# Kernel optimization log

Measured on AMD Instinct MI355X. Metric: run time of the kernel, lower is better.

The kernel has to match this reference:

```python
import jax, jax.numpy as jnp
import numpy as np

UNITS = 256
INNER_ITERS = 1
INNER_LR = [0.01]
LN_EPS = 1e-3  # keras LayerNormalization default epsilon
B, L, F = 512, 128, 128


def _encoder(W1, b1, W2, b2, z):
    # keras 'gelu' activation is exact (approximate=False)
    h = jax.nn.gelu(z @ W1 + b1, approximate=False)
    return h @ W2 + b2


def _layer_norm(z, g, b):
    m = jnp.mean(z, axis=-1, keepdims=True)
    v = jnp.var(z, axis=-1, keepdims=True)
    return g * (z - m) / jnp.sqrt(v + LN_EPS) + b


def setup_inputs():
    U = UNITS
    key = jax.random.key(0)
    ks = jax.random.split(key, 12)
    s = 0.02
    return {
        "inputs": jax.random.normal(ks[0], (B, F), jnp.float32),
        "prev_hidden": jax.random.normal(ks[1], (B, U), jnp.float32),
        "sequence_buffer": jax.random.normal(ks[2], (B, L, U), jnp.float32),
        "Wp": jax.random.normal(ks[3], (F, U)) * s, "bp": jnp.zeros((U,)),
        "Wphi": jax.random.normal(ks[4], (U, U)) * s, "bphi": jnp.zeros((U,)),
        "Wpsi": jax.random.normal(ks[5], (U, U)) * s, "bpsi": jnp.zeros((U,)),
        "W1": jax.random.normal(ks[6], (U, 4 * U)) * s, "b1": jnp.zeros((4 * U,)),
        "W2": jax.random.normal(ks[7], (4 * U, U)) * s, "b2": jnp.zeros((U,)),
        "Wg": jax.random.normal(ks[8], (U, U)) * s, "g_bias": jnp.zeros((U,)),
        "ln_g": jnp.ones((U,)), "ln_b": jnp.zeros((U,)),
        "Wh": jax.random.normal(ks[9], (U, U)) * s, "h_bias": jnp.zeros((U,)),
    }


def reference(inputs, prev_hidden, sequence_buffer, Wp, bp, Wphi, bphi, Wpsi, bpsi,
              W1, b1, W2, b2, Wg, g_bias, ln_g, ln_b, Wh, h_bias):
    U = UNITS
    bsz = inputs.shape[0]
    # input projection (F != units)
    proj = inputs @ Wp + bp                                   # [B, U]
    # shift buffer, append projected input
    buf = jnp.concatenate([sequence_buffer[:, 1:, :], proj[:, None, :]], axis=1)  # [B, L, U]
    x = buf[:, :-1, :].reshape(-1, U)                         # [B*(L-1), U]
    y = buf[:, 1:, :].reshape(-1, U)
    phi = x @ Wphi + bphi

    params = (W1, b1, W2, b2)

    def inner_loss(p):
        rec = _layer_norm(_encoder(*p, phi) @ Wg + g_bias, ln_g, ln_b)
        return jnp.mean(jnp.square(rec - y)), rec

    rec = None
    for it in range(INNER_ITERS):
        (_, rec), grads = jax.value_and_grad(inner_loss, has_aux=True)(params)
        lr = INNER_LR[min(it, len(INNER_LR) - 1)]
        params = tuple(p - lr * g for p, g in zip(params, grads))

    psi = buf[:, -1, :] @ Wpsi + bpsi                         # [B, U]
    contrib = jnp.mean(rec.reshape(bsz, -1, U), axis=1)       # [B, U]
    # psi path uses the UPDATED inner-encoder weights
    out = (_encoder(*params, psi) + contrib) @ Wh + h_bias    # [B, U]
    return out, buf
```

## Files before the change

### kernel.cpp

```cpp
#include <hip/hip_runtime.h>
#include <cmath>

typedef __bf16 bf16;
typedef __attribute__((ext_vector_type(8))) __bf16 bf16x8;
typedef __attribute__((ext_vector_type(4))) __bf16 bf16x4v;
typedef __attribute__((ext_vector_type(4))) float f32x4;
typedef __attribute__((ext_vector_type(2))) unsigned int u32x2;

constexpr int NROWS = 512 * 127;
constexpr float LR = 0.01f;
constexpr float INV_NU = 1.f / (65024.f * 256.f);

__device__ __forceinline__ float sigf(float x) {
  return 1.f / (1.f + __expf(-1.702f * x));
}
__device__ __forceinline__ float gelu_fast(float x) { return x * sigf(x); }
__device__ __forceinline__ float dgelu_fast(float x) {
  float s = sigf(x);
  return s * (1.f + 1.702f * x * (1.f - s));
}
__device__ __forceinline__ bf16x8 gelu8f(bf16x8 v) {
  bf16x8 o;
#pragma unroll
  for (int i = 0; i < 8; i++) o[i] = (bf16)gelu_fast((float)v[i]);
  return o;
}

__device__ __forceinline__ void gload16(const bf16* g, const bf16* lds) {
  __builtin_amdgcn_global_load_lds(
      (const __attribute__((address_space(1))) unsigned int*)(size_t)(const void*)g,
      (__attribute__((address_space(3))) unsigned int*)(unsigned)(size_t)(const void*)lds,
      16, 0, 0);
}

__device__ __forceinline__ int xcd_lin() {
  int p = ((int)blockIdx.z * (int)gridDim.y + (int)blockIdx.y) * (int)gridDim.x + (int)blockIdx.x;
  const int total = (int)gridDim.x * (int)gridDim.y * (int)gridDim.z;
  if (!(total & 7)) p = (p & 7) * (total >> 3) + (p >> 3);
  return p;
}

template <int EPI>
__global__ __launch_bounds__(256, 4) void gemm6_k(
    const bf16* __restrict__ A, const bf16* __restrict__ Bt,
    const float* __restrict__ bias, void* __restrict__ out0,
    void* __restrict__ out1, const bf16* __restrict__ aux,
    int M, int N, int K) {
  __shared__ __align__(16) bf16 As[2][128 * 32];
  __shared__ __align__(16) bf16 Bs[2][128 * 32];
  const int t = threadIdx.x;
  const int p = xcd_lin();
  const int bn = (p % (int)gridDim.x) * 128;
  const int bm = (p / (int)gridDim.x) * 128;
  const int lane = t & 63, w = t >> 6;
  const int wr = w >> 1, wc = w & 1;

  f32x4 acc[4][4];
#pragma unroll
  for (int mi = 0; mi < 4; mi++)
#pragma unroll
    for (int ni = 0; ni < 4; ni++) {
      f32x4 z = {0.f, 0.f, 0.f, 0.f};
      acc[mi][ni] = z;
    }

  const int lr = lane >> 2;
  const int csw = (lane & 3) ^ (lr & 3);
  const bf16* aBase = A + (size_t)(bm + 32 * w + lr) * K + csw * 8;
  const bf16* bBase = Bt + (size_t)(bn + 32 * w + lr) * K + csw * 8;

  const int ml = lane & 15, g = lane >> 4;
  const int c0 = g ^ (ml & 3);

  const int nt = K >> 5;
#pragma unroll
  for (int i = 0; i < 2; i++) {
    gload16(aBase + (size_t)(16 * i) * K, As[0] + (32 * w + 16 * i) * 32);
    gload16(bBase + (size_t)(16 * i) * K, Bs[0] + (32 * w + 16 * i) * 32);
  }

  for (int tt = 0; tt < nt; tt++) {
    const int cur = tt & 1;
    if (tt + 1 < nt) {
      const int ko = (tt + 1) * 32;
#pragma unroll
      for (int i = 0; i < 2; i++) {
        gload16(aBase + (size_t)(16 * i) * K + ko, As[cur ^ 1] + (32 * w + 16 * i) * 32);
        gload16(bBase + (size_t)(16 * i) * K + ko, Bs[cur ^ 1] + (32 * w + 16 * i) * 32);
      }
      asm volatile("s_waitcnt vmcnt(4)" ::: "memory");
    } else {
      asm volatile("s_waitcnt vmcnt(0)" ::: "memory");
    }
    __builtin_amdgcn_s_barrier();
    __builtin_amdgcn_sched_barrier(0);

    bf16x8 af[4], bfr[4];
#pragma unroll
    for (int mi = 0; mi < 4; mi++) {
      const int m = wr * 64 + mi * 16 + ml;
      const int n = wc * 64 + mi * 16 + ml;
      af[mi] = *(const bf16x8*)&As[cur][m * 32 + c0 * 8];
      bfr[mi] = *(const bf16x8*)&Bs[cur][n * 32 + c0 * 8];
    }
#pragma unroll
    for (int mi = 0; mi < 4; mi++)
#pragma unroll
      for (int ni = 0; ni < 4; ni++)
        acc[mi][ni] = __builtin_amdgcn_mfma_f32_16x16x32_bf16(
            bfr[ni], af[mi], acc[mi][ni], 0, 0, 0);
    __builtin_amdgcn_s_barrier();
  }

  const int g4 = (lane >> 4) << 2;
#pragma unroll
  for (int mi = 0; mi < 4; mi++) {
    const int m = bm + wr * 64 + mi * 16 + ml;
#pragma unroll
    for (int ni = 0; ni < 4; ni++) {
      const int n0 = bn + wc * 64 + ni * 16 + g4;
      f32x4 v = acc[mi][ni];
      if (bias) {
        const float4 bv = *(const float4*)(bias + n0);
        v[0] += bv.x; v[1] += bv.y; v[2] += bv.z; v[3] += bv.w;
      }
      const size_t idx = (size_t)m * N + n0;
      if constexpr (EPI == 0) {
        *(float4*)((float*)out0 + idx) = make_float4(v[0], v[1], v[2], v[3]);
      } else if constexpr (EPI == 1) {
        bf16x4v o;
#pragma unroll
        for (int j = 0; j < 4; j++) o[j] = (bf16)v[j];
        *(bf16x4v*)((bf16*)out0 + idx) = o;
      } else if constexpr (EPI == 2) {
        bf16x4v od, oh;
#pragma unroll
        for (int j = 0; j < 4; j++) {
          float s = sigf(v[j]);
          oh[j] = (bf16)(v[j] * s);
          od[j] = (bf16)(s * (1.f + 1.702f * v[j] * (1.f - s)));
        }
        *(bf16x4v*)((bf16*)out0 + idx) = od;
        *(bf16x4v*)((bf16*)out1 + idx) = oh;
      } else if constexpr (EPI == 3) {
        bf16x4v o;
#pragma unroll
        for (int j = 0; j < 4; j++) o[j] = (bf16)gelu_fast(v[j]);
        *(bf16x4v*)((bf16*)out0 + idx) = o;
      } else if constexpr (EPI == 5) {
        const bf16x4v a4 = *(const bf16x4v*)(aux + idx);
        bf16x4v o;
#pragma unroll
        for (int j = 0; j < 4; j++) o[j] = (bf16)(v[j] * dgelu_fast((float)a4[j]));
        *(bf16x4v*)((bf16*)out0 + idx) = o;
      } else if constexpr (EPI == 6) {
        const bf16x4v a4 = *(const bf16x4v*)(aux + idx);
        bf16x4v o;
#pragma unroll
        for (int j = 0; j < 4; j++) o[j] = (bf16)(v[j] * (float)a4[j]);
        *(bf16x4v*)((bf16*)out0 + idx) = o;
      } else if constexpr (EPI == 7) {
        *(float4*)((float*)out0 + idx) = make_float4(v[0], v[1], v[2], v[3]);
        bf16x4v o;
#pragma unroll
        for (int j = 0; j < 4; j++) o[j] = (bf16)v[j];
        *(bf16x4v*)((bf16*)out1 + idx) = o;
      } else {
        const float4 c4 = *(const float4*)((const float*)aux + idx);
        bf16x4v o;
        o[0] = (bf16)(v[0] + c4.x); o[1] = (bf16)(v[1] + c4.y);
        o[2] = (bf16)(v[2] + c4.z); o[3] = (bf16)(v[3] + c4.w);
        *(bf16x4v*)((bf16*)out0 + idx) = o;
      }
    }
  }
}

template <int EPI, bool GA>
__global__ __launch_bounds__(256) void gemm_k(
    const bf16* __restrict__ A, const bf16* __restrict__ Bt,
    const float* __restrict__ bias, void* __restrict__ out0,
    void* __restrict__ out1, const bf16* __restrict__ aux,
    int M, int N, int K) {
  __shared__ bf16 As[128][40];
  __shared__ bf16 Bs[128][40];
  const int t = threadIdx.x;
  const int bm = blockIdx.x * 128, bn = blockIdx.y * 128;
  const int lane = t & 63, w = t >> 6;
  const int wr = w >> 1, wc = w & 1;

  f32x4 acc[4][4];
#pragma unroll
  for (int mi = 0; mi < 4; mi++)
#pragma unroll
    for (int ni = 0; ni < 4; ni++) {
      f32x4 z = {0.f, 0.f, 0.f, 0.f};
      acc[mi][ni] = z;
    }
  const int r2 = t >> 2;
  const int c8 = (t & 3) * 8;

  for (int kt = 0; kt < K; kt += 32) {
    __syncthreads();
    {
      bf16x8 a0 = *(const bf16x8*)(A + (size_t)(bm + r2) * K + kt + c8);
      bf16x8 a1 = *(const bf16x8*)(A + (size_t)(bm + r2 + 64) * K + kt + c8);
      bf16x8 b0 = *(const bf16x8*)(Bt + (size_t)(bn + r2) * K + kt + c8);
      bf16x8 b1 = *(const bf16x8*)(Bt + (size_t)(bn + r2 + 64) * K + kt + c8);
      if constexpr (GA) { a0 = gelu8f(a0); a1 = gelu8f(a1); }
      *(bf16x8*)&As[r2][c8] = a0;
      *(bf16x8*)&As[r2 + 64][c8] = a1;
      *(bf16x8*)&Bs[r2][c8] = b0;
      *(bf16x8*)&Bs[r2 + 64][c8] = b1;
    }
    __syncthreads();
    bf16x8 af[4], bfr[4];
#pragma unroll
    for (int mi = 0; mi < 4; mi++)
      af[mi] = *(const bf16x8*)&As[wr * 64 + mi * 16 + (lane & 15)][(lane >> 4) * 8];
#pragma unroll
    for (int ni = 0; ni < 4; ni++)
      bfr[ni] = *(const bf16x8*)&Bs[wc * 64 + ni * 16 + (lane & 15)][(lane >> 4) * 8];
#pragma unroll
    for (int mi = 0; mi < 4; mi++)
#pragma unroll
      for (int ni = 0; ni < 4; ni++)
        acc[mi][ni] = __builtin_amdgcn_mfma_f32_16x16x32_bf16(af[mi], bfr[ni], acc[mi][ni], 0, 0, 0);
  }

#pragma unroll
  for (int ni = 0; ni < 4; ni++) {
    const int col = bn + wc * 64 + ni * 16 + (lane & 15);
    const float bv = bias ? bias[col] : 0.f;
#pragma unroll
    for (int mi = 0; mi < 4; mi++) {
      const int rb = bm + wr * 64 + mi * 16 + ((lane >> 4) << 2);
#pragma unroll
      for (int r = 0; r < 4; r++) {
        float v = acc[mi][ni][r] + bv;
        size_t idx = (size_t)(rb + r) * N + col;
        if constexpr (EPI == 1) {
          ((bf16*)out0)[idx] = (bf16)v;
        } else {
          ((float*)out0)[idx] = v;
        }
      }
    }
  }
}

template <bool GELU_A>
__global__ __launch_bounds__(256) void tgemm4_k(
    const bf16* __restrict__ Asrc, const bf16* __restrict__ Bsrc,
    float* __restrict__ outP, int M, int N, int ldA, int ldB, int K) {
  __shared__ __align__(16) bf16 As[2][4736];
  __shared__ __align__(16) bf16 Bs[2][4736];
  const int t = threadIdx.x;
  const int p = xcd_lin();
  const int gx = (int)gridDim.x, gy = (int)gridDim.y;
  const int bm = (p % gx) * 128;
  const int bn = ((p / gx) % gy) * 128;
  const int zc = p / (gx * gy);
  const int r0 = zc * 1024;
  const int rows = (K - r0 < 1024) ? (K - r0) : 1024;
  const int nt = rows >> 5;
  const int lane = t & 63, w = t >> 6, wr = w >> 1, wc = w & 1;

  f32x4 acc[4][4];
#pragma unroll
  for (int mi = 0; mi < 4; mi++)
#pragma unroll
    for (int ni = 0; ni < 4; ni++) {
      f32x4 z = {0.f, 0.f, 0.f, 0.f};
      acc[mi][ni] = z;
    }

  const bool isB = t >= 128;
  const int srow = (t & 127) >> 4;
  const int scol = (t & 15) * 8;
  const int sms = (t & 15) >> 1;
  const int shalf = (t & 1) * 8;
  const bf16* src = isB ? Bsrc : Asrc;
  const int ld = isB ? ldB : ldA;
  const int bx = isB ? bn : bm;
  const int sidx = sms * 592 + srow * 16 + shalf;

  const unsigned abase = (unsigned)(size_t)(void*)As;
  const unsigned bbase = (unsigned)(size_t)(void*)Bs;
  const int g = lane >> 4;
  const int ml = lane & 15;
  const unsigned acol0 = abase + 2u * (unsigned)((wr * 4) * 592 + g * 144 + ml);
  const unsigned bcol0 = bbase + 2u * (unsigned)((wc * 4) * 592 + g * 144 + ml);

  auto ldrow = [&](int kt, int ll) {
    return *(const bf16x8*)(src + (size_t)(r0 + kt + srow + ll * 8) * ld + bx + scol);
  };
  auto wrbuf = [&](bf16* dst, bf16x8* stg) {
#pragma unroll
    for (int ll = 0; ll < 4; ll++) {
      bf16x8 v = stg[ll];
      if constexpr (GELU_A) { if (!isB) v = gelu8f(v); }
      *(bf16x8*)&dst[sidx + ll * 144] = v;
    }
  };

  bf16x8 stg[4];
#pragma unroll
  for (int ll = 0; ll < 4; ll++) stg[ll] = ldrow(0, ll);
  wrbuf(isB ? Bs[0] : As[0], stg);
  __syncthreads();

  for (int tt = 0; tt < nt; tt++) {
    const int cur = tt & 1;
    if (tt + 1 < nt) {
#pragma unroll
      for (int ll = 0; ll < 4; ll++) stg[ll] = ldrow((tt + 1) * 32, ll);
    }
    const unsigned boff = (unsigned)cur * (4736u * 2u);
    union FR { u32x2 pr[2]; bf16x8 v; };
    FR af[4], bfr[4];
#pragma unroll
    for (int mi = 0; mi < 4; mi++) {
      const unsigned a = acol0 + boff + (unsigned)(mi * 1184);
      asm volatile("ds_read_b64_tr_b16 %0, %1" : "=v"(af[mi].pr[0]) : "v"(a));
      asm volatile("ds_read_b64_tr_b16 %0, %1 offset:128" : "=v"(af[mi].pr[1]) : "v"(a));
    }
#pragma unroll
    for (int ni = 0; ni < 4; ni++) {
      const unsigned b = bcol0 + boff + (unsigned)(ni * 1184);
      asm volatile("ds_read_b64_tr_b16 %0, %1" : "=v"(bfr[ni].pr[0]) : "v"(b));
      asm volatile("ds_read_b64_tr_b16 %0, %1 offset:128" : "=v"(bfr[ni].pr[1]) : "v"(b));
    }
    asm volatile("s_waitcnt lgkmcnt(0)" ::: "memory");
    __builtin_amdgcn_sched_barrier(0);

#pragma unroll
    for (int mi = 0; mi < 4; mi++)
#pragma unroll
      for (int ni = 0; ni < 4; ni++)
        acc[mi][ni] = __builtin_amdgcn_mfma_f32_16x16x32_bf16(
            bfr[ni].v, af[mi].v, acc[mi][ni], 0, 0, 0);

    if (tt + 1 < nt) wrbuf(isB ? Bs[cur ^ 1] : As[cur ^ 1], stg);
    __syncthreads();
  }

  float* o = outP + (size_t)zc * M * N;
  const int g4 = (lane >> 4) << 2;
#pragma unroll
  for (int mi = 0; mi < 4; mi++) {
    const int m = bm + wr * 64 + mi * 16 + ml;
#pragma unroll
    for (int ni = 0; ni < 4; ni++) {
      const int n0 = bn + wc * 64 + ni * 16 + g4;
      f32x4 v = acc[mi][ni];
      *(float4*)(o + (size_t)m * N + n0) = make_float4(v[0], v[1], v[2], v[3]);
    }
  }
}

__global__ void prep_k(const float* inputs, const float* Wp, const float* Wphi,
                       const float* W1, const float* W2, const float* Wg,
                       const float* Wpsi, const float* Wh,
                       bf16* inb, bf16* WpT, bf16* WphiT, bf16* W1T, bf16* W2T,
                       bf16* WgT, bf16* Wgb, bf16* W2b, bf16* WpsiT, bf16* WhT) {
  int i = blockIdx.x * 256 + threadIdx.x;
  if (i < 65536) {
    inb[i] = (bf16)inputs[i];
  } else if ((i -= 65536) < 32768) {
    int u = i >> 7, f = i & 127;
    WpT[i] = (bf16)Wp[f * 256 + u];
  } else if ((i -= 32768) < 65536) {
    int n = i >> 8, k = i & 255;
    WphiT[i] = (bf16)Wphi[k * 256 + n];
  } else if ((i -= 65536) < 262144) {
    int h = i >> 8, u = i & 255;
    W1T[i] = (bf16)W1[u * 1024 + h];
  } else if ((i -= 262144) < 262144) {
    int u = i >> 10, h = i & 1023;
    W2T[i] = (bf16)W2[h * 256 + u];
  } else if ((i -= 262144) < 65536) {
    int n = i >> 8, k = i & 255;
    WgT[i] = (bf16)Wg[k * 256 + n];
  } else if ((i -= 65536) < 65536) {
    Wgb[i] = (bf16)Wg[i];
  } else if ((i -= 65536) < 262144) {
    W2b[i] = (bf16)W2[i];
  } else if ((i -= 262144) < 65536) {
    int n = i >> 8, k = i & 255;
    WpsiT[i] = (bf16)Wpsi[k * 256 + n];
  } else if ((i -= 65536) < 65536) {
    int n = i >> 8, k = i & 255;
    WhT[i] = (bf16)Wh[k * 256 + n];
  }
}

__global__ void bzg_k(const float* __restrict__ b2, const float* __restrict__ Wg,
                      const float* __restrict__ gbias, float* __restrict__ bzg) {
  const int n = threadIdx.x;
  float s = gbias[n];
  for (int j = 0; j < 256; j++) s += b2[j] * Wg[j * 256 + n];
  bzg[n] = s;
}

__global__ void xcast_k(const float* __restrict__ seq, bf16* __restrict__ xb) {
  int v8 = blockIdx.x * 256 + threadIdx.x;
  int r = v8 >> 5, c8 = (v8 & 31) * 8;
  int b = r / 127, t = r - b * 127;
  const float* src = seq + ((size_t)(b * 128 + t + 1)) * 256 + c8;
  float4 v0 = *(const float4*)(src);
  float4 v1 = *(const float4*)(src + 4);
  bf16x8 o;
  o[0] = (bf16)v0.x; o[1] = (bf16)v0.y; o[2] = (bf16)v0.z; o[3] = (bf16)v0.w;
  o[4] = (bf16)v1.x; o[5] = (bf16)v1.y; o[6] = (bf16)v1.z; o[7] = (bf16)v1.w;
  *(bf16x8*)(xb + (size_t)r * 256 + c8) = o;
}

__global__ void bufwrite_k(const float* __restrict__ seq, const float* __restrict__ proj,
                           float* __restrict__ buf) {
  int i = blockIdx.x * 256 + threadIdx.x;
  int b = i >> 13, rem = i & 8191;
  int j = rem >> 6, c4 = (rem & 63) * 4;
  float4 v;
  if (j < 127)
    v = *(const float4*)(seq + ((size_t)(b * 128 + j + 1)) * 256 + c4);
  else
    v = *(const float4*)(proj + (size_t)b * 256 + c4);
  *(float4*)(buf + ((size_t)(b * 128 + j)) * 256 + c4) = v;
}

__global__ __launch_bounds__(256) void ln_k(const bf16* zin, bf16* dzout,
                                            const float* __restrict__ seq,
                                            const float* __restrict__ proj,
                                            const float* __restrict__ lng,
                                            const float* __restrict__ lnb,
                                            bf16* __restrict__ rec) {
  const int w = threadIdx.x >> 6, lane = threadIdx.x & 63;
  const int r = blockIdx.x * 4 + w;
  const int b = r / 127, tt = r - b * 127;
  typedef __attribute__((ext_vector_type(4))) __bf16 bf16x4;
  bf16x4 zv = *(const bf16x4*)(zin + (size_t)r * 256 + lane * 4);
  float z0 = (float)zv[0], z1 = (float)zv[1], z2 = (float)zv[2], z3 = (float)zv[3];
  float s1 = z0 + z1 + z2 + z3;
  float s2 = z0 * z0 + z1 * z1 + z2 * z2 + z3 * z3;
  for (int m = 1; m < 64; m <<= 1) { s1 += __shfl_xor(s1, m); s2 += __shfl_xor(s2, m); }
  const float mean = s1 * (1.f / 256.f);
  const float var = s2 * (1.f / 256.f) - mean * mean;
  const float rs = rsqrtf(var + 1e-3f);
  const float4 gv = *(const float4*)(lng + lane * 4);
  const float4 bv = *(const float4*)(lnb + lane * 4);
  const float* ysrc = (tt < 126) ? (seq + ((size_t)(b * 128 + tt + 2)) * 256)
                                 : (proj + (size_t)b * 256);
  const float4 yv = *(const float4*)(ysrc + lane * 4);
  float xh0 = (z0 - mean) * rs, xh1 = (z1 - mean) * rs, xh2 = (z2 - mean) * rs, xh3 = (z3 - mean) * rs;
  float r0 = gv.x * xh0 + bv.x, r1 = gv.y * xh1 + bv.y, r2 = gv.z * xh2 + bv.z, r3 = gv.w * xh3 + bv.w;
  float u0 = 2.f * (r0 - yv.x) * INV_NU * gv.x;
  float u1 = 2.f * (r1 - yv.y) * INV_NU * gv.y;
  float u2 = 2.f * (r2 - yv.z) * INV_NU * gv.z;
  float u3 = 2.f * (r3 - yv.w) * INV_NU * gv.w;
  float t1 = u0 + u1 + u2 + u3;
  float t2 = u0 * xh0 + u1 * xh1 + u2 * xh2 + u3 * xh3;
  for (int m = 1; m < 64; m <<= 1) { t1 += __shfl_xor(t1, m); t2 += __shfl_xor(t2, m); }
  const float mu = t1 * (1.f / 256.f), mux = t2 * (1.f / 256.f);
  bf16x4 ro, dzo;
  ro[0] = (bf16)r0; ro[1] = (bf16)r1; ro[2] = (bf16)r2; ro[3] = (bf16)r3;
  dzo[0] = (bf16)((u0 - mu - xh0 * mux) * rs);
  dzo[1] = (bf16)((u1 - mu - xh1 * mux) * rs);
  dzo[2] = (bf16)((u2 - mu - xh2 * mux) * rs);
  dzo[3] = (bf16)((u3 - mu - xh3 * mux) * rs);
  *(bf16x4*)(rec + (size_t)r * 256 + lane * 4) = ro;
  *(bf16x4*)(dzout + (size_t)r * 256 + lane * 4) = dzo;
}

__global__ void colsum_k(const bf16* __restrict__ src, float* __restrict__ part, int C) {
  const int col = blockIdx.x * 256 + threadIdx.x;
  const int ch = blockIdx.y;
  float s = 0.f;
  const int rbeg = ch * 1016;
  for (int rr = rbeg; rr < rbeg + 1016; rr++) s += (float)src[(size_t)rr * C + col];
  part[(size_t)ch * C + col] = s;
}

__global__ void contrib_k(const bf16* __restrict__ rec, float* __restrict__ contrib) {
  const int b = blockIdx.x, u = threadIdx.x;
  float s = 0.f;
  for (int t = 0; t < 127; t++) s += (float)rec[((size_t)b * 127 + t) * 256 + u];
  contrib[b * 256 + u] = s * (1.f / 127.f);
}

__global__ void update2_k(const float* __restrict__ pW2, const float* __restrict__ pdb2,
                          const float* __restrict__ W2, const float* __restrict__ b2,
                          bf16* __restrict__ W2pT, float* __restrict__ b2p) {
  int idx = blockIdx.x * 256 + threadIdx.x;
  if (idx < 262144) {
    float s = 0.f;
    for (int z = 0; z < 64; z++) s += pW2[(size_t)z * 262144 + idx];
    int h = idx >> 8, u = idx & 255;
    W2pT[(size_t)u * 1024 + h] = (bf16)(W2[idx] - LR * s);
  } else {
    int u = idx - 262144;
    float s = 0.f;
    for (int c = 0; c < 64; c++) s += pdb2[c * 256 + u];
    b2p[u] = b2[u] - LR * s;
  }
}

__global__ void update1_k(const float* __restrict__ pW1, const float* __restrict__ pdb1,
                          const float* __restrict__ W1, const float* __restrict__ b1,
                          bf16* __restrict__ W1pT, float* __restrict__ b1p) {
  int idx = blockIdx.x * 256 + threadIdx.x;
  if (idx < 262144) {
    float s = 0.f;
    for (int z = 0; z < 64; z++) s += pW1[(size_t)z * 262144 + idx];
    int u = idx >> 10, h = idx & 1023;
    W1pT[(size_t)h * 256 + u] = (bf16)(W1[idx] - LR * s);
  } else {
    int h = idx - 262144;
    float s = 0.f;
    for (int c = 0; c < 64; c++) s += pdb1[c * 1024 + h];
    b1p[h] = b1[h] - LR * s;
  }
}

extern "C" void kernel_launch(void* const* d_in, const int* in_sizes, int n_in,
                              void* d_out, int out_size, void* d_ws, size_t ws_size,
                              hipStream_t stream) {
  const float* inputs = (const float*)d_in[0];
  const float* seq = (const float*)d_in[2];
  const float* Wp = (const float*)d_in[3];
  const float* bp = (const float*)d_in[4];
  const float* Wphi = (const float*)d_in[5];
  const float* bphi = (const float*)d_in[6];
  const float* Wpsi = (const float*)d_in[7];
  const float* bpsi = (const float*)d_in[8];
  const float* W1 = (const float*)d_in[9];
  const float* b1 = (const float*)d_in[10];
  const float* W2 = (const float*)d_in[11];
  const float* b2 = (const float*)d_in[12];
  const float* Wg = (const float*)d_in[13];
  const float* gbias = (const float*)d_in[14];
  const float* lng = (const float*)d_in[15];
  const float* lnb = (const float*)d_in[16];
  const float* Wh = (const float*)d_in[17];
  const float* hbias = (const float*)d_in[18];

  float* out = (float*)d_out;
  float* buf = out + 131072;
  float* pW2 = buf;
  float* pW1 = buf;

  char* wptr = (char*)d_ws;
  auto alloc = [&](size_t bytes) {
    char* p = wptr;
    wptr += (bytes + 255) & ~(size_t)255;
    return p;
  };
  bf16* inb   = (bf16*)alloc(65536 * 2);
  bf16* WpT   = (bf16*)alloc(32768 * 2);
  bf16* WphiT = (bf16*)alloc(65536 * 2);
  bf16* W1T   = (bf16*)alloc(262144 * 2);
  bf16* W2T   = (bf16*)alloc(262144 * 2);
  bf16* WgT   = (bf16*)alloc(65536 * 2);
  bf16* Wgb   = (bf16*)alloc(65536 * 2);
  bf16* W2b   = (bf16*)alloc(262144 * 2);
  bf16* WpsiT = (bf16*)alloc(65536 * 2);
  bf16* WhT   = (bf16*)alloc(65536 * 2);
  bf16* WzgT  = (bf16*)alloc(262144 * 2);
  float* bzg  = (float*)alloc(256 * 4);
  bf16* W1pT  = (bf16*)alloc(262144 * 2);
  bf16* W2pT  = (bf16*)alloc(262144 * 2);
  float* b1p  = (float*)alloc(1024 * 4);
  float* b2p  = (float*)alloc(256 * 4);
  float* proj = (float*)alloc(131072 * 4);
  bf16* projb = (bf16*)alloc(131072 * 2);
  float* pdb2 = (float*)alloc(64 * 256 * 4);
  float* pdb1 = (float*)alloc(64 * 1024 * 4);
  bf16* psib  = (bf16*)alloc(131072 * 2);
  bf16* hpb   = (bf16*)alloc(524288 * 2);
  float* contrib = (float*)alloc(131072 * 4);
  bf16* finb  = (bf16*)alloc(131072 * 2);
  const size_t NU = (size_t)NROWS * 256;
  const size_t NH = (size_t)NROWS * 1024;
  bf16* xz     = (bf16*)alloc(NU * 2);
  bf16* phi    = (bf16*)alloc(NU * 2);
  bf16* a1b    = (bf16*)alloc(NH * 2);
  bf16* encden = (bf16*)alloc(NU * 2);
  const bool useH = ws_size >= (size_t)((char*)wptr - (char*)d_ws) + NH * 2 + 4096;
  bf16* hbuf = useH ? (bf16*)alloc(NH * 2) : nullptr;

  prep_k<<<4736, 256, 0, stream>>>(inputs, Wp, Wphi, W1, W2, Wg, Wpsi, Wh,
                                   inb, WpT, WphiT, W1T, W2T, WgT, Wgb, W2b, WpsiT, WhT);
  gemm6_k<1><<<dim3(8, 2), 256, 0, stream>>>(WgT, W2b, nullptr, WzgT, nullptr, nullptr, 256, 1024, 256);
  bzg_k<<<1, 256, 0, stream>>>(b2, Wg, gbias, bzg);
  xcast_k<<<8128, 256, 0, stream>>>(seq, xz);
  gemm6_k<7><<<dim3(2, 4), 256, 0, stream>>>(inb, WpT, bp, proj, projb, nullptr, 512, 256, 128);
  gemm6_k<1><<<dim3(2, 508), 256, 0, stream>>>(xz, WphiT, bphi, phi, nullptr, nullptr, NROWS, 256, 256);
  if (useH)
    gemm6_k<2><<<dim3(8, 508), 256, 0, stream>>>(phi, W1T, b1, a1b, hbuf, nullptr, NROWS, 1024, 256);
  else
    gemm6_k<1><<<dim3(8, 508), 256, 0, stream>>>(phi, W1T, b1, a1b, nullptr, nullptr, NROWS, 1024, 256);
  if (useH)
    gemm6_k<1><<<dim3(2, 508), 256, 0, stream>>>(hbuf, WzgT, bzg, xz, nullptr, nullptr, NROWS, 256, 1024);
  else
    gemm_k<1, true><<<dim3(508, 2), 256, 0, stream>>>(a1b, WzgT, bzg, xz, nullptr, nullptr, NROWS, 256, 1024);
  ln_k<<<16256, 256, 0, stream>>>(xz, xz, seq, proj, lng, lnb, encden);
  contrib_k<<<512, 256, 0, stream>>>(encden, contrib);
  gemm6_k<1><<<dim3(2, 508), 256, 0, stream>>>(xz, Wgb, nullptr, encden, nullptr, nullptr, NROWS, 256, 256);
  colsum_k<<<dim3(1, 64), 256, 0, stream>>>(encden, pdb2, 256);
  if (useH)
    tgemm4_k<false><<<dim3(8, 2, 64), 256, 0, stream>>>(hbuf, encden, pW2, 1024, 256, 1024, 256, NROWS);
  else
    tgemm4_k<true><<<dim3(8, 2, 64), 256, 0, stream>>>(a1b, encden, pW2, 1024, 256, 1024, 256, NROWS);
  update2_k<<<1025, 256, 0, stream>>>(pW2, pdb2, W2, b2, W2pT, b2p);
  if (useH)
    gemm6_k<6><<<dim3(8, 508), 256, 0, stream>>>(encden, W2b, nullptr, a1b, nullptr, a1b, NROWS, 1024, 256);
  else
    gemm6_k<5><<<dim3(8, 508), 256, 0, stream>>>(encden, W2b, nullptr, a1b, nullptr, a1b, NROWS, 1024, 256);
  colsum_k<<<dim3(4, 64), 256, 0, stream>>>(a1b, pdb1, 1024);
  tgemm4_k<false><<<dim3(2, 8, 64), 256, 0, stream>>>(phi, a1b, pW1, 256, 1024, 256, 1024, NROWS);
  update1_k<<<1028, 256, 0, stream>>>(pW1, pdb1, W1, b1, W1pT, b1p);
  bufwrite_k<<<16384, 256, 0, stream>>>(seq, proj, buf);
  gemm6_k<1><<<dim3(2, 4), 256, 0, stream>>>(projb, WpsiT, bpsi, psib, nullptr, nullptr, 512, 256, 256);
  gemm6_k<3><<<dim3(8, 4), 256, 0, stream>>>(psib, W1pT, b1p, hpb, nullptr, nullptr, 512, 1024, 256);
  gemm6_k<8><<<dim3(2, 4), 256, 0, stream>>>(hpb, W2pT, b2p, finb, nullptr, (const bf16*)contrib, 512, 256, 1024);
  gemm6_k<0><<<dim3(2, 4), 256, 0, stream>>>(finb, WhT, hbias, out, nullptr, nullptr, 512, 256, 256);
}
```

Measured before the change: 889.7 us.

## Drop materialized GELU buffer; fuse GELU into pipelined Zg GEMM load

Removes the optional separate GELU activation buffer (hbuf) and its extra 65024x1024 bf16 write and reads. GELU is recomputed on the fly when loading A tiles, both in a new double-buffered, swizzled GEMM kernel for the Wzg projection and in the weight-gradient GEMM. The new kernel also uses an XCD-aware block order, async B loads and vectorized epilogue stores. It saves memory traffic at the cost of recomputing GELU twice per element.

```diff
diff --git a/kernel.cpp b/kernel.cpp
--- a/kernel.cpp
+++ b/kernel.cpp
@@ -176,16 +176,18 @@
   }
 }
 
-template <int EPI, bool GA>
-__global__ __launch_bounds__(256) void gemm_k(
+template <int EPI>
+__global__ __launch_bounds__(256, 4) void gemm7_k(
     const bf16* __restrict__ A, const bf16* __restrict__ Bt,
     const float* __restrict__ bias, void* __restrict__ out0,
     void* __restrict__ out1, const bf16* __restrict__ aux,
     int M, int N, int K) {
-  __shared__ bf16 As[128][40];
-  __shared__ bf16 Bs[128][40];
+  __shared__ __align__(16) bf16 As[2][128 * 32];
+  __shared__ __align__(16) bf16 Bs[2][128 * 32];
   const int t = threadIdx.x;
-  const int bm = blockIdx.x * 128, bn = blockIdx.y * 128;
+  const int p = xcd_lin();
+  const int bn = (p % (int)gridDim.x) * 128;
+  const int bm = (p / (int)gridDim.x) * 128;
   const int lane = t & 63, w = t >> 6;
   const int wr = w >> 1, wc = w & 1;
 
@@ -197,53 +199,80 @@
       f32x4 z = {0.f, 0.f, 0.f, 0.f};
       acc[mi][ni] = z;
     }
-  const int r2 = t >> 2;
-  const int c8 = (t & 3) * 8;
-
-  for (int kt = 0; kt < K; kt += 32) {
+
+  const int lr = lane >> 2;
+  const int csw = (lane & 3) ^ (lr & 3);
+  const bf16* aBase = A + (size_t)(bm + 32 * w + lr) * K + csw * 8;
+  const bf16* bBase = Bt + (size_t)(bn + 32 * w + lr) * K + csw * 8;
+  const int awoff = (32 * w + lr) * 32 + (lane & 3) * 8;
+
+  const int ml = lane & 15, g = lane >> 4;
+  const int c0 = g ^ (ml & 3);
+
+  const int nt = K >> 5;
+  {
+    bf16x8 av0 = *(const bf16x8*)aBase;
+    bf16x8 av1 = *(const bf16x8*)(aBase + (size_t)16 * K);
+    gload16(bBase, Bs[0] + (32 * w) * 32);
+    gload16(bBase + (size_t)16 * K, Bs[0] + (32 * w + 16) * 32);
+    *(bf16x8*)&As[0][awoff] = gelu8f(av0);
+    *(bf16x8*)&As[0][awoff + 512] = gelu8f(av1);
+  }
+  __syncthreads();
+
+  bf16x8 av0, av1;
+  for (int tt = 0; tt < nt; tt++) {
+    const int cur = tt & 1;
+    if (tt + 1 < nt) {
+      const int ko = (tt + 1) * 32;
+      gload16(bBase + ko, Bs[cur ^ 1] + (32 * w) * 32);
+      gload16(bBase + (size_t)16 * K + ko, Bs[cur ^ 1] + (32 * w + 16) * 32);
+      av0 = *(const bf16x8*)(aBase + ko);
+      av1 = *(const bf16x8*)(aBase + (size_t)16 * K + ko);
+    }
+
+    bf16x8 af[4], bfr[4];
+#pragma unroll
+    for (int mi = 0; mi < 4; mi++) {
+      const int m = wr * 64 + mi * 16 + ml;
+      const int n = wc * 64 + mi * 16 + ml;
+      af[mi] = *(const bf16x8*)&As[cur][m * 32 + c0 * 8];
+      bfr[mi] = *(const bf16x8*)&Bs[cur][n * 32 + c0 * 8];
+    }
+#pragma unroll
+    for (int mi = 0; mi < 4; mi++)
+#pragma unroll
+      for (int ni = 0; ni < 4; ni++)
+        acc[mi][ni] = __builtin_amdgcn_mfma_f32_16x16x32_bf16(
+            bfr[ni], af[mi], acc[mi][ni], 0, 0, 0);
+
+    if (tt + 1 < nt) {
+      *(bf16x8*)&As[cur ^ 1][awoff] = gelu8f(av0);
+      *(bf16x8*)&As[cur ^ 1][awoff + 512] = gelu8f(av1);
+    }
     __syncthreads();
-    {
-      bf16x8 a0 = *(const bf16x8*)(A + (size_t)(bm + r2) * K + kt + c8);
-      bf16x8 a1 = *(const bf16x8*)(A + (size_t)(bm + r2 + 64) * K + kt + c8);
-      bf16x8 b0 = *(const bf16x8*)(Bt + (size_t)(bn + r2) * K + kt + c8);
-      bf16x8 b1 = *(const bf16x8*)(Bt + (size_t)(bn + r2 + 64) * K + kt + c8);
-      if constexpr (GA) { a0 = gelu8f(a0); a1 = gelu8f(a1); }
-      *(bf16x8*)&As[r2][c8] = a0;
-      *(bf16x8*)&As[r2 + 64][c8] = a1;
-      *(bf16x8*)&Bs[r2][c8] = b0;
-      *(bf16x8*)&Bs[r2 + 64][c8] = b1;
-    }
-    __syncthreads();
-    bf16x8 af[4], bfr[4];
-#pragma unroll
-    for (int mi = 0; mi < 4; mi++)
-      af[mi] = *(const bf16x8*)&As[wr * 64 + mi * 16 + (lane & 15)][(lane >> 4) * 8];
-#pragma unroll
-    for (int ni = 0; ni < 4; ni++)
-      bfr[ni] = *(const bf16x8*)&Bs[wc * 64 + ni * 16 + (lane & 15)][(lane >> 4) * 8];
-#pragma unroll
-    for (int mi = 0; mi < 4; mi++)
-#pragma unroll
-      for (int ni = 0; ni < 4; ni++)
-        acc[mi][ni] = __builtin_amdgcn_mfma_f32_16x16x32_bf16(af[mi], bfr[ni], acc[mi][ni], 0, 0, 0);
-  }
-
-#pragma unroll
-  for (int ni = 0; ni < 4; ni++) {
-    const int col = bn + wc * 64 + ni * 16 + (lane & 15);
-    const float bv = bias ? bias[col] : 0.f;
-#pragma unroll
-    for (int mi = 0; mi < 4; mi++) {
-      const int rb = bm + wr * 64 + mi * 16 + ((lane >> 4) << 2);
-#pragma unroll
-      for (int r = 0; r < 4; r++) {
-        float v = acc[mi][ni][r] + bv;
-        size_t idx = (size_t)(rb + r) * N + col;
-        if constexpr (EPI == 1) {
-          ((bf16*)out0)[idx] = (bf16)v;
-        } else {
-          ((float*)out0)[idx] = v;
-        }
+  }
+
+  const int g4 = (lane >> 4) << 2;
+#pragma unroll
+  for (int mi = 0; mi < 4; mi++) {
+    const int m = bm + wr * 64 + mi * 16 + ml;
+#pragma unroll
+    for (int ni = 0; ni < 4; ni++) {
+      const int n0 = bn + wc * 64 + ni * 16 + g4;
+      f32x4 v = acc[mi][ni];
+      if (bias) {
+        const float4 bv = *(const float4*)(bias + n0);
+        v[0] += bv.x; v[1] += bv.y; v[2] += bv.z; v[3] += bv.w;
+      }
+      const size_t idx = (size_t)m * N + n0;
+      if constexpr (EPI == 0) {
+        *(float4*)((float*)out0 + idx) = make_float4(v[0], v[1], v[2], v[3]);
+      } else {
+        bf16x4v o;
+#pragma unroll
+        for (int j = 0; j < 4; j++) o[j] = (bf16)v[j];
+        *(bf16x4v*)((bf16*)out0 + idx) = o;
       }
     }
   }
@@ -585,8 +614,6 @@
   bf16* phi    = (bf16*)alloc(NU * 2);
   bf16* a1b    = (bf16*)alloc(NH * 2);
   bf16* encden = (bf16*)alloc(NU * 2);
-  const bool useH = ws_size >= (size_t)((char*)wptr - (char*)d_ws) + NH * 2 + 4096;
-  bf16* hbuf = useH ? (bf16*)alloc(NH * 2) : nullptr;
 
   prep_k<<<4736, 256, 0, stream>>>(inputs, Wp, Wphi, W1, W2, Wg, Wpsi, Wh,
                                    inb, WpT, WphiT, W1T, W2T, WgT, Wgb, W2b, WpsiT, WhT);
@@ -595,27 +622,15 @@
   xcast_k<<<8128, 256, 0, stream>>>(seq, xz);
   gemm6_k<7><<<dim3(2, 4), 256, 0, stream>>>(inb, WpT, bp, proj, projb, nullptr, 512, 256, 128);
   gemm6_k<1><<<dim3(2, 508), 256, 0, stream>>>(xz, WphiT, bphi, phi, nullptr, nullptr, NROWS, 256, 256);
-  if (useH)
-    gemm6_k<2><<<dim3(8, 508), 256, 0, stream>>>(phi, W1T, b1, a1b, hbuf, nullptr, NROWS, 1024, 256);
-  else
-    gemm6_k<1><<<dim3(8, 508), 256, 0, stream>>>(phi, W1T, b1, a1b, nullptr, nullptr, NROWS, 1024, 256);
-  if (useH)
-    gemm6_k<1><<<dim3(2, 508), 256, 0, stream>>>(hbuf, WzgT, bzg, xz, nullptr, nullptr, NROWS, 256, 1024);
-  else
-    gemm_k<1, true><<<dim3(508, 2), 256, 0, stream>>>(a1b, WzgT, bzg, xz, nullptr, nullptr, NROWS, 256, 1024);
+  gemm6_k<1><<<dim3(8, 508), 256, 0, stream>>>(phi, W1T, b1, a1b, nullptr, nullptr, NROWS, 1024, 256);
+  gemm7_k<1><<<dim3(2, 508), 256, 0, stream>>>(a1b, WzgT, bzg, xz, nullptr, nullptr, NROWS, 256, 1024);
   ln_k<<<16256, 256, 0, stream>>>(xz, xz, seq, proj, lng, lnb, encden);
   contrib_k<<<512, 256, 0, stream>>>(encden, contrib);
   gemm6_k<1><<<dim3(2, 508), 256, 0, stream>>>(xz, Wgb, nullptr, encden, nullptr, nullptr, NROWS, 256, 256);
   colsum_k<<<dim3(1, 64), 256, 0, stream>>>(encden, pdb2, 256);
-  if (useH)
-    tgemm4_k<false><<<dim3(8, 2, 64), 256, 0, stream>>>(hbuf, encden, pW2, 1024, 256, 1024, 256, NROWS);
-  else
-    tgemm4_k<true><<<dim3(8, 2, 64), 256, 0, stream>>>(a1b, encden, pW2, 1024, 256, 1024, 256, NROWS);
+  tgemm4_k<true><<<dim3(8, 2, 64), 256, 0, stream>>>(a1b, encden, pW2, 1024, 256, 1024, 256, NROWS);
   update2_k<<<1025, 256, 0, stream>>>(pW2, pdb2, W2, b2, W2pT, b2p);
-  if (useH)
-    gemm6_k<6><<<dim3(8, 508), 256, 0, stream>>>(encden, W2b, nullptr, a1b, nullptr, a1b, NROWS, 1024, 256);
-  else
-    gemm6_k<5><<<dim3(8, 508), 256, 0, stream>>>(encden, W2b, nullptr, a1b, nullptr, a1b, NROWS, 1024, 256);
+  gemm6_k<5><<<dim3(8, 508), 256, 0, stream>>>(encden, W2b, nullptr, a1b, nullptr, a1b, NROWS, 1024, 256);
   colsum_k<<<dim3(4, 64), 256, 0, stream>>>(a1b, pdb1, 1024);
   tgemm4_k<false><<<dim3(2, 8, 64), 256, 0, stream>>>(phi, a1b, pW1, 256, 1024, 256, 1024, NROWS);
   update1_k<<<1028, 256, 0, stream>>>(pW1, pdb1, W1, b1, W1pT, b1p);
```

Measured after the change: 862.3 us. -3.1%, faster.
